# Kernel optimization log

Measured on AMD Instinct MI355X. Metric: run time of the kernel, lower is better.

Reference implementation:

```python
import jax, jax.numpy as jnp
import numpy as np

N = 50000      # nodes
IN = 128       # in_channels
H = 8          # heads
C = 16         # out_channels per head (128 // 8)
E = 800000     # edges per relation
R = 2          # number of relations
NEG_SLOPE = 0.2


def setup_inputs() -> dict:
    key = jax.random.key(0)
    ks = jax.random.split(key, 6)
    x = jax.random.normal(ks[0], (N, IN), jnp.float32)
    edge_index0 = jax.random.randint(ks[1], (2, E), 0, N, jnp.int32)
    edge_index1 = jax.random.randint(ks[2], (2, E), 0, N, jnp.int32)
    s_in = np.float32(1.0 / np.sqrt(IN))
    Wl = jax.random.normal(ks[3], (R, IN, H * C), jnp.float32) * s_in
    Wr = jax.random.normal(ks[4], (R, IN, H * C), jnp.float32) * s_in
    att = jax.random.normal(ks[5], (R, H, C), jnp.float32) * np.float32(1.0 / np.sqrt(C))
    bl = jnp.zeros((R, H * C), jnp.float32)
    br = jnp.zeros((R, H * C), jnp.float32)
    bias = jnp.zeros((R, H * C), jnp.float32)
    return dict(x=x, edge_index0=edge_index0, edge_index1=edge_index1,
                Wl=Wl, bl=bl, Wr=Wr, br=br, att=att, bias=bias)


def _gatv2_conv(x, edge_index, Wl, bl, Wr, br, att, bias):
    """One PyG-style GATv2Conv (share_weights=False, add_self_loops=True, concat=True)."""
    loops = jnp.arange(N, dtype=edge_index.dtype)
    src = jnp.concatenate([edge_index[0], loops])  # [E+N]
    dst = jnp.concatenate([edge_index[1], loops])  # [E+N]
    xl = (x @ Wl + bl).reshape(N, H, C)  # source-side transform (messages)
    xr = (x @ Wr + br).reshape(N, H, C)  # destination-side transform
    # GATv2 attention: att . leaky_relu(x_l[src] + x_r[dst])
    e = jax.nn.leaky_relu(xl[src] + xr[dst], NEG_SLOPE)        # [E+N, H, C]
    score = jnp.einsum('ehc,hc->eh', e, att)                   # [E+N, H]
    # per-destination softmax (numerically stable via segment max)
    m = jax.ops.segment_max(score, dst, num_segments=N)        # [N, H]
    m = jax.lax.stop_gradient(jnp.where(jnp.isfinite(m), m, jnp.zeros_like(m)))
    ex = jnp.exp(score - m[dst])
    den = jax.ops.segment_sum(ex, dst, num_segments=N)         # [N, H]
    alpha = ex / den[dst]                                      # [E+N, H]
    # scatter-add weighted source messages
    out = jax.ops.segment_sum(alpha[:, :, None] * xl[src], dst, num_segments=N)  # [N, H, C]
    return out.reshape(N, H * C) + bias


def reference(x, edge_index0, edge_index1, Wl, bl, Wr, br, att, bias):
    eis = (edge_index0, edge_index1)
    out = jnp.zeros((N, H * C), x.dtype)
    for r in range(R):  # small fixed loop over relation types
        out = out + _gatv2_conv(x, eis[r], Wl[r], bl[r], Wr[r], br[r], att[r], bias[r])
    return out
```

## Files before the change

### kernel.cpp

```cpp
#include <hip/hip_runtime.h>
#include <math.h>

#define NN 50000
#define EE 800000
#define NB 196
#define BCAP 6250
#define LCAP 32

typedef __attribute__((ext_vector_type(8))) short bf16x8;
typedef __attribute__((ext_vector_type(4))) float f32x4;

__device__ inline uint bfpack(float a, float b) {
    uint ua = __float_as_uint(a); ua = (ua + 0x7FFFu + ((ua >> 16) & 1u)) >> 16;
    uint ub = __float_as_uint(b); ub = (ub + 0x7FFFu + ((ub >> 16) & 1u)) >> 16;
    return ua | (ub << 16);
}

__global__ __launch_bounds__(256) void k_prep(
    const float* __restrict__ x, const float* __restrict__ Wl, const float* __restrict__ Wr,
    ushort* __restrict__ xb, ushort* __restrict__ wt, int* __restrict__ gcur)
{
    int i = blockIdx.x * 256 + threadIdx.x;
    if (i < NN * 32) {
        float4 v = ((const float4*)x)[i];
        uint2 p; p.x = bfpack(v.x, v.y); p.y = bfpack(v.z, v.w);
        ((uint2*)xb)[i] = p;
    }
    if (i < 4 * 16384) {
        int c = i >> 14, rem = i & 16383, nn = rem >> 7, k = rem & 127;
        const float* W = ((c & 1) ? Wr : Wl) + (c >> 1) * 16384;
        float v = W[k * 128 + nn];
        uint u = __float_as_uint(v); u = (u + 0x7FFFu + ((u >> 16) & 1u)) >> 16;
        wt[c * 16384 + nn * 128 + k] = (ushort)u;
    }
    if (i < 2 * 256 * 16) gcur[i] = 0;
}

__global__ __launch_bounds__(256) void k_gemm_all(
    const ushort* __restrict__ xb, const ushort* __restrict__ wt,
    const float* __restrict__ bl, const float* __restrict__ br,
    ushort* __restrict__ xall)
{
    const int c = blockIdx.y;
    const ushort* __restrict__ w = wt + c * 16384;
    const float* __restrict__ bv = ((c & 1) ? br : bl) + (c >> 1) * 128;
    ushort* __restrict__ outp = xall + (size_t)c * NN * 128;

    const int wid = threadIdx.x >> 6, lane = threadIdx.x & 63;
    const int hi = lane >> 4, lo = lane & 15;
    const int row = blockIdx.x * 64 + wid * 16 + lo;
    const int rc = (row < NN) ? row : NN - 1;

    f32x4 acc[8];
    #pragma unroll
    for (int tt = 0; tt < 8; ++tt) acc[tt] = (f32x4){0.f, 0.f, 0.f, 0.f};

    #pragma unroll
    for (int kk = 0; kk < 128; kk += 32) {
        bf16x8 bfr = *(const bf16x8*)&xb[(size_t)rc * 128 + kk + hi * 8];
        #pragma unroll
        for (int tt = 0; tt < 8; ++tt) {
            bf16x8 afr = *(const bf16x8*)&w[(tt * 16 + lo) * 128 + kk + hi * 8];
            acc[tt] = __builtin_amdgcn_mfma_f32_16x16x32_bf16(afr, bfr, acc[tt], 0, 0, 0);
        }
    }
    if (row < NN) {
        #pragma unroll
        for (int tt = 0; tt < 8; ++tt) {
            float4 bvv = *(const float4*)&bv[tt * 16 + hi * 4];
            uint2 pk;
            pk.x = bfpack(acc[tt][0] + bvv.x, acc[tt][1] + bvv.y);
            pk.y = bfpack(acc[tt][2] + bvv.z, acc[tt][3] + bvv.w);
            *(uint2*)&outp[(size_t)row * 128 + tt * 16 + hi * 4] = pk;
        }
    }
}

__global__ __launch_bounds__(256) void k_bin1(
    const int* __restrict__ ei0, const int* __restrict__ ei1,
    int* __restrict__ gcur, uint* __restrict__ gbuf)
{
    const int rel = blockIdx.y;
    const int* __restrict__ ei = rel ? ei1 : ei0;
    int* __restrict__ gc = gcur + rel * 256 * 16;
    uint* __restrict__ gb = gbuf + (size_t)rel * 256 * BCAP;

    __shared__ uint stage[256 * LCAP];
    __shared__ int scnt[256];
    const int tid = threadIdx.x;
    scnt[tid] = 0;
    __syncthreads();

    const int base = blockIdx.x * 2048;
    uint keys[8]; int bk[8];
    #pragma unroll
    for (int k = 0; k < 8; ++k) {
        int e = base + tid + k * 256;
        bool v = (e < EE);
        int d = v ? ei[EE + e] : 0;
        int s = v ? ei[e] : 0;
        keys[k] = ((uint)d << 16) | (uint)s;
        bk[k] = v ? (d >> 8) : -1;
    }
    #pragma unroll
    for (int k = 0; k < 8; ++k) {
        if (bk[k] >= 0) {
            int pos = atomicAdd(&scnt[bk[k]], 1);
            if (pos < LCAP) stage[bk[k] * LCAP + pos] = keys[k];
            else {
                int gpos = atomicAdd(&gc[bk[k] * 16], 1);
                if (gpos < BCAP) gb[bk[k] * BCAP + gpos] = keys[k];
            }
        }
    }
    __syncthreads();
    int c = scnt[tid]; if (c > LCAP) c = LCAP;
    if (c > 0) {
        int b0 = atomicAdd(&gc[tid * 16], c);
        if (b0 + c > BCAP) c = (b0 < BCAP) ? (BCAP - b0) : 0;
        for (int i = 0; i < c; ++i) gb[tid * BCAP + b0 + i] = stage[tid * LCAP + i];
    }
}

__global__ __launch_bounds__(256) void k_bin2(
    const int* __restrict__ gcur, const uint* __restrict__ gbuf,
    ushort* __restrict__ bin0, ushort* __restrict__ bin1,
    int* __restrict__ cur0, int* __restrict__ cur1)
{
    const int rel = blockIdx.y;
    const int b = blockIdx.x;
    const int* __restrict__ gc = gcur + rel * 256 * 16;
    const uint* __restrict__ gb = gbuf + (size_t)rel * 256 * BCAP + (size_t)b * BCAP;
    ushort* __restrict__ bins = rel ? bin1 : bin0;
    int* __restrict__ cur = rel ? cur1 : cur0;

    __shared__ int cnt[256];
    cnt[threadIdx.x] = 0;
    __syncthreads();
    int n = gc[b * 16]; if (n > BCAP) n = BCAP;
    for (int i = threadIdx.x; i < n; i += 256) {
        uint key = gb[i];
        int d = key >> 16;
        int pos = atomicAdd(&cnt[d & 255], 1);
        if (pos < 64) bins[(size_t)d * 64 + pos] = (ushort)(key & 0xFFFF);
    }
    __syncthreads();
    int gd = (b << 8) + threadIdx.x;
    if (gd < NN) cur[gd] = cnt[threadIdx.x];
}

__global__ __launch_bounds__(256) void k_gat(
    const ushort* __restrict__ xall,
    const int* __restrict__ cur0, const int* __restrict__ cur1,
    const ushort* __restrict__ bin0, const ushort* __restrict__ bin1,
    const float* __restrict__ att, const float* __restrict__ bias,
    float* __restrict__ out)
{
    const int wid  = threadIdx.x >> 6;
    const int lane = threadIdx.x & 63;
    const int li   = lane & 31;
    const int half = lane >> 5;
    const int d = blockIdx.x * 4 + wid;

    const uint2* __restrict__ x2 = (const uint2*)xall;
    const size_t hb = (size_t)(half * 2) * NN * 32;
    const size_t rb = (size_t)(half * 2 + 1) * NN * 32;

    float4 av = *(const float4*)&att[half * 128 + li * 4];
    uint2 ur = x2[rb + (size_t)d * 32 + li];
    float r0 = __uint_as_float(ur.x << 16), r1 = __uint_as_float(ur.x & 0xFFFF0000u);
    float r2 = __uint_as_float(ur.y << 16), r3 = __uint_as_float(ur.y & 0xFFFF0000u);

    int nb = (half ? cur1 : cur0)[d]; nb = (nb > 64) ? 64 : nb;
    const int n = nb + 1;
    int nm = n;
    nm = max(nm, __shfl_xor(nm, 32));
    const ushort* __restrict__ brow = (half ? bin1 : bin0) + (size_t)d * 64;

    auto sidx = [&](int e) -> int {
        int ec = (e < n) ? e : (n - 1);
        return (ec == 0) ? d : (int)brow[ec - 1];
    };

    uint2 u0 = x2[hb + (size_t)sidx(0) * 32 + li];
    uint2 u1 = x2[hb + (size_t)sidx(1) * 32 + li];
    int   s2 = sidx(2);

    float a0 = 0.f, a1 = 0.f, a2 = 0.f, a3 = 0.f, den = 0.f;
    for (int t = 0; t < nm; ++t) {
        uint2 cu = u0;
        u0 = u1;
        u1 = x2[hb + (size_t)s2 * 32 + li];
        s2 = sidx(t + 3);
        float c0 = __uint_as_float(cu.x << 16), c1 = __uint_as_float(cu.x & 0xFFFF0000u);
        float c2 = __uint_as_float(cu.y << 16), c3 = __uint_as_float(cu.y & 0xFFFF0000u);
        float q0 = c0 + r0, q1 = c1 + r1, q2 = c2 + r2, q3 = c3 + r3;
        q0 = fmaxf(q0, 0.2f * q0); q1 = fmaxf(q1, 0.2f * q1);
        q2 = fmaxf(q2, 0.2f * q2); q3 = fmaxf(q3, 0.2f * q3);
        float p = av.x * q0 + av.y * q1 + av.z * q2 + av.w * q3;
        p += __shfl_xor(p, 1);
        p += __shfl_xor(p, 2);
        float ex = (t < n) ? __expf(p) : 0.f;
        a0 += ex * c0; a1 += ex * c1; a2 += ex * c2; a3 += ex * c3; den += ex;
    }
    float inv = 1.f / den;
    float b0 = a0 * inv, b1 = a1 * inv, b2 = a2 * inv, b3 = a3 * inv;
    b0 += __shfl_xor(b0, 32);
    b1 += __shfl_xor(b1, 32);
    b2 += __shfl_xor(b2, 32);
    b3 += __shfl_xor(b3, 32);
    if (half == 0) {
        float4 bb0 = *(const float4*)&bias[li * 4];
        float4 bb1 = *(const float4*)&bias[128 + li * 4];
        float4 o;
        o.x = bb0.x + bb1.x + b0; o.y = bb0.y + bb1.y + b1;
        o.z = bb0.z + bb1.z + b2; o.w = bb0.w + bb1.w + b3;
        *(float4*)&out[(size_t)d * 128 + li * 4] = o;
    }
}

extern "C" void kernel_launch(void* const* d_in, const int* in_sizes, int n_in,
                              void* d_out, int out_size, void* d_ws, size_t ws_size,
                              hipStream_t stream) {
    (void)in_sizes; (void)n_in; (void)out_size; (void)ws_size;
    const float* x    = (const float*)d_in[0];
    const int*   ei0  = (const int*)  d_in[1];
    const int*   ei1  = (const int*)  d_in[2];
    const float* Wl   = (const float*)d_in[3];
    const float* bl   = (const float*)d_in[4];
    const float* Wr   = (const float*)d_in[5];
    const float* br   = (const float*)d_in[6];
    const float* att  = (const float*)d_in[7];
    const float* bias = (const float*)d_in[8];
    float* out = (float*)d_out;

    ushort* xb   = (ushort*)d_ws;
    uint*   gbuf = (uint*)d_ws;
    ushort* wt   = xb + (size_t)NN * 128;
    ushort* xall = wt + 4 * 16384;
    ushort* bin0 = xall + (size_t)4 * NN * 128;
    ushort* bin1 = bin0 + (size_t)NN * 64;
    int* cur0 = (int*)(bin1 + (size_t)NN * 64);
    int* cur1 = cur0 + NN;
    int* gcur = cur1 + NN;

    k_prep<<<(NN * 32 + 255) / 256, 256, 0, stream>>>(x, Wl, Wr, xb, wt, gcur);
    k_gemm_all<<<dim3((NN + 63) / 64, 4), 256, 0, stream>>>(xb, wt, bl, br, xall);
    k_bin1<<<dim3((EE + 2047) / 2048, 2), 256, 0, stream>>>(ei0, ei1, gcur, gbuf);
    k_bin2<<<dim3(NB, 2), 256, 0, stream>>>(gcur, gbuf, bin0, bin1, cur0, cur1);
    k_gat<<<NN / 4, 256, 0, stream>>>(xall, cur0, cur1, bin0, bin1, att, bias, out);
}
```

Before: 265.3 us.

## Fuse x conversion into GEMM, precompute attention dots, simplify GAT score math

Converts x to bf16 inside the GEMM instead of in a separate prep pass, and has the GEMM also emit per-head att·x dot products. The GAT kernel splits leaky_relu into a linear part taken from the precomputed dots plus an abs term, and uses exp2 with folded log2e constants and 32-bit index arithmetic. The bin flush in k_bin1 becomes wave-cooperative, with one atomic per bucket and parallel lane writes. This adds an extra dotv gather per edge and a larger workspace footprint.

```diff
diff --git a/kernel.cpp b/kernel.cpp
--- a/kernel.cpp
+++ b/kernel.cpp
@@ -15,17 +15,14 @@
     uint ub = __float_as_uint(b); ub = (ub + 0x7FFFu + ((ub >> 16) & 1u)) >> 16;
     return ua | (ub << 16);
 }
+__device__ inline float bflo(uint u) { return __uint_as_float(u << 16); }
+__device__ inline float bfhi(uint u) { return __uint_as_float(u & 0xFFFF0000u); }
 
 __global__ __launch_bounds__(256) void k_prep(
-    const float* __restrict__ x, const float* __restrict__ Wl, const float* __restrict__ Wr,
-    ushort* __restrict__ xb, ushort* __restrict__ wt, int* __restrict__ gcur)
+    const float* __restrict__ Wl, const float* __restrict__ Wr,
+    ushort* __restrict__ wt, int* __restrict__ gcur)
 {
     int i = blockIdx.x * 256 + threadIdx.x;
-    if (i < NN * 32) {
-        float4 v = ((const float4*)x)[i];
-        uint2 p; p.x = bfpack(v.x, v.y); p.y = bfpack(v.z, v.w);
-        ((uint2*)xb)[i] = p;
-    }
     if (i < 4 * 16384) {
         int c = i >> 14, rem = i & 16383, nn = rem >> 7, k = rem & 127;
         const float* W = ((c & 1) ? Wr : Wl) + (c >> 1) * 16384;
@@ -37,14 +34,17 @@
 }
 
 __global__ __launch_bounds__(256) void k_gemm_all(
-    const ushort* __restrict__ xb, const ushort* __restrict__ wt,
+    const float* __restrict__ x, const ushort* __restrict__ wt,
     const float* __restrict__ bl, const float* __restrict__ br,
-    ushort* __restrict__ xall)
+    const float* __restrict__ att,
+    ushort* __restrict__ xall, float* __restrict__ dotv)
 {
     const int c = blockIdx.y;
     const ushort* __restrict__ w = wt + c * 16384;
     const float* __restrict__ bv = ((c & 1) ? br : bl) + (c >> 1) * 128;
+    const float* __restrict__ attp = att + (c >> 1) * 128;
     ushort* __restrict__ outp = xall + (size_t)c * NN * 128;
+    float* __restrict__ dvp = dotv + (size_t)c * NN * 8;
 
     const int wid = threadIdx.x >> 6, lane = threadIdx.x & 63;
     const int hi = lane >> 4, lo = lane & 15;
@@ -57,7 +57,12 @@
 
     #pragma unroll
     for (int kk = 0; kk < 128; kk += 32) {
-        bf16x8 bfr = *(const bf16x8*)&xb[(size_t)rc * 128 + kk + hi * 8];
+        const float4* xp = (const float4*)&x[(size_t)rc * 128 + kk + hi * 8];
+        float4 f0 = xp[0], f1 = xp[1];
+        uint4 px;
+        px.x = bfpack(f0.x, f0.y); px.y = bfpack(f0.z, f0.w);
+        px.z = bfpack(f1.x, f1.y); px.w = bfpack(f1.z, f1.w);
+        bf16x8 bfr = *(bf16x8*)&px;
         #pragma unroll
         for (int tt = 0; tt < 8; ++tt) {
             bf16x8 afr = *(const bf16x8*)&w[(tt * 16 + lo) * 128 + kk + hi * 8];
@@ -72,6 +77,12 @@
             pk.x = bfpack(acc[tt][0] + bvv.x, acc[tt][1] + bvv.y);
             pk.y = bfpack(acc[tt][2] + bvv.z, acc[tt][3] + bvv.w);
             *(uint2*)&outp[(size_t)row * 128 + tt * 16 + hi * 4] = pk;
+            float w0 = bflo(pk.x), w1 = bfhi(pk.x), w2 = bflo(pk.y), w3 = bfhi(pk.y);
+            float4 a4 = *(const float4*)&attp[tt * 16 + hi * 4];
+            float s = a4.x * w0 + a4.y * w1 + a4.z * w2 + a4.w * w3;
+            s += __shfl_xor(s, 16);
+            s += __shfl_xor(s, 32);
+            if (hi == 0) dvp[(size_t)row * 8 + tt] = s;
         }
     }
 }
@@ -114,11 +125,19 @@
         }
     }
     __syncthreads();
-    int c = scnt[tid]; if (c > LCAP) c = LCAP;
-    if (c > 0) {
-        int b0 = atomicAdd(&gc[tid * 16], c);
-        if (b0 + c > BCAP) c = (b0 < BCAP) ? (BCAP - b0) : 0;
-        for (int i = 0; i < c; ++i) gb[tid * BCAP + b0 + i] = stage[tid * LCAP + i];
+    const int wv = tid >> 6, ln = tid & 63;
+    #pragma unroll 4
+    for (int g = 0; g < 64; ++g) {
+        int b = wv * 64 + g;
+        int cnum = scnt[b]; if (cnum > LCAP) cnum = LCAP;
+        if (cnum == 0) continue;
+        int b0 = 0;
+        if (ln == 0) b0 = atomicAdd(&gc[b * 16], cnum);
+        b0 = __shfl(b0, 0);
+        if (ln < cnum) {
+            int idx = b0 + ln;
+            if (idx < BCAP) gb[b * BCAP + idx] = stage[b * LCAP + ln];
+        }
     }
 }
 
@@ -150,7 +169,7 @@
 }
 
 __global__ __launch_bounds__(256) void k_gat(
-    const ushort* __restrict__ xall,
+    const ushort* __restrict__ xall, const float* __restrict__ dotv,
     const int* __restrict__ cur0, const int* __restrict__ cur1,
     const ushort* __restrict__ bin0, const ushort* __restrict__ bin1,
     const float* __restrict__ att, const float* __restrict__ bias,
@@ -160,16 +179,24 @@
     const int lane = threadIdx.x & 63;
     const int li   = lane & 31;
     const int half = lane >> 5;
+    const int h    = li >> 2;
     const int d = blockIdx.x * 4 + wid;
 
     const uint2* __restrict__ x2 = (const uint2*)xall;
-    const size_t hb = (size_t)(half * 2) * NN * 32;
-    const size_t rb = (size_t)(half * 2 + 1) * NN * 32;
-
+    const uint hb = (uint)(half * 2) * (NN * 32);
+    const uint rb = hb + NN * 32;
+    const float* __restrict__ dAp = dotv + (size_t)(half * 2) * NN * 8;
+    const float* __restrict__ dBp = dAp + (size_t)NN * 8;
+
+    const float L2E = 1.4426950408889634f;
+    const float C6 = 0.6f * L2E;
     float4 av = *(const float4*)&att[half * 128 + li * 4];
-    uint2 ur = x2[rb + (size_t)d * 32 + li];
-    float r0 = __uint_as_float(ur.x << 16), r1 = __uint_as_float(ur.x & 0xFFFF0000u);
-    float r2 = __uint_as_float(ur.y << 16), r3 = __uint_as_float(ur.y & 0xFFFF0000u);
+    const float k4 = 0.4f * L2E;
+    float avx = av.x * k4, avy = av.y * k4, avz = av.z * k4, avw = av.w * k4;
+
+    uint2 ur = x2[rb + (uint)d * 32 + li];
+    float r0 = bflo(ur.x), r1 = bfhi(ur.x), r2 = bflo(ur.y), r3 = bfhi(ur.y);
+    float dBk = C6 * dBp[(uint)d * 8 + h];
 
     int nb = (half ? cur1 : cur0)[d]; nb = (nb > 64) ? 64 : nb;
     const int n = nb + 1;
@@ -182,26 +209,33 @@
         return (ec == 0) ? d : (int)brow[ec - 1];
     };
 
-    uint2 u0 = x2[hb + (size_t)sidx(0) * 32 + li];
-    uint2 u1 = x2[hb + (size_t)sidx(1) * 32 + li];
-    int   s2 = sidx(2);
+    int s0i = sidx(0), s1i = sidx(1);
+    uint2 u0 = x2[hb + (uint)s0i * 32 + li];
+    float g0 = dAp[(uint)s0i * 8 + h];
+    uint2 u1 = x2[hb + (uint)s1i * 32 + li];
+    float g1 = dAp[(uint)s1i * 8 + h];
+    int s2 = sidx(2);
 
     float a0 = 0.f, a1 = 0.f, a2 = 0.f, a3 = 0.f, den = 0.f;
     for (int t = 0; t < nm; ++t) {
-        uint2 cu = u0;
-        u0 = u1;
-        u1 = x2[hb + (size_t)s2 * 32 + li];
+        uint2 cu = u0; float cg = g0;
+        u0 = u1; g0 = g1;
+        u1 = x2[hb + (uint)s2 * 32 + li];
+        g1 = dAp[(uint)s2 * 8 + h];
         s2 = sidx(t + 3);
-        float c0 = __uint_as_float(cu.x << 16), c1 = __uint_as_float(cu.x & 0xFFFF0000u);
-        float c2 = __uint_as_float(cu.y << 16), c3 = __uint_as_float(cu.y & 0xFFFF0000u);
+        float c0 = bflo(cu.x), c1 = bfhi(cu.x), c2 = bflo(cu.y), c3 = bfhi(cu.y);
         float q0 = c0 + r0, q1 = c1 + r1, q2 = c2 + r2, q3 = c3 + r3;
-        q0 = fmaxf(q0, 0.2f * q0); q1 = fmaxf(q1, 0.2f * q1);
-        q2 = fmaxf(q2, 0.2f * q2); q3 = fmaxf(q3, 0.2f * q3);
-        float p = av.x * q0 + av.y * q1 + av.z * q2 + av.w * q3;
-        p += __shfl_xor(p, 1);
-        p += __shfl_xor(p, 2);
-        float ex = (t < n) ? __expf(p) : 0.f;
-        a0 += ex * c0; a1 += ex * c1; a2 += ex * c2; a3 += ex * c3; den += ex;
+        float m = avx * fabsf(q0);
+        m = fmaf(avy, fabsf(q1), m);
+        m = fmaf(avz, fabsf(q2), m);
+        m = fmaf(avw, fabsf(q3), m);
+        m += __shfl_xor(m, 1);
+        m += __shfl_xor(m, 2);
+        float p = m + fmaf(C6, cg, dBk);
+        float ex = (t < n) ? __builtin_amdgcn_exp2f(p) : 0.f;
+        a0 = fmaf(ex, c0, a0); a1 = fmaf(ex, c1, a1);
+        a2 = fmaf(ex, c2, a2); a3 = fmaf(ex, c3, a3);
+        den += ex;
     }
     float inv = 1.f / den;
     float b0 = a0 * inv, b1 = a1 * inv, b2 = a2 * inv, b3 = a3 * inv;
@@ -234,19 +268,19 @@
     const float* bias = (const float*)d_in[8];
     float* out = (float*)d_out;
 
-    ushort* xb   = (ushort*)d_ws;
-    uint*   gbuf = (uint*)d_ws;
-    ushort* wt   = xb + (size_t)NN * 128;
-    ushort* xall = wt + 4 * 16384;
-    ushort* bin0 = xall + (size_t)4 * NN * 128;
+    ushort* xall = (ushort*)d_ws;
+    float*  dotv = (float*)(xall + (size_t)4 * NN * 128);
+    uint*   gbuf = (uint*)(dotv + (size_t)4 * NN * 8);
+    ushort* wt   = (ushort*)(gbuf + (size_t)2 * 256 * BCAP);
+    ushort* bin0 = wt + 4 * 16384;
     ushort* bin1 = bin0 + (size_t)NN * 64;
     int* cur0 = (int*)(bin1 + (size_t)NN * 64);
     int* cur1 = cur0 + NN;
     int* gcur = cur1 + NN;
 
-    k_prep<<<(NN * 32 + 255) / 256, 256, 0, stream>>>(x, Wl, Wr, xb, wt, gcur);
-    k_gemm_all<<<dim3((NN + 63) / 64, 4), 256, 0, stream>>>(xb, wt, bl, br, xall);
+    k_prep<<<256, 256, 0, stream>>>(Wl, Wr, wt, gcur);
+    k_gemm_all<<<dim3((NN + 63) / 64, 4), 256, 0, stream>>>(x, wt, bl, br, att, xall, dotv);
     k_bin1<<<dim3((EE + 2047) / 2048, 2), 256, 0, stream>>>(ei0, ei1, gcur, gbuf);
     k_bin2<<<dim3(NB, 2), 256, 0, stream>>>(gcur, gbuf, bin0, bin1, cur0, cur1);
-    k_gat<<<NN / 4, 256, 0, stream>>>(xall, cur0, cur1, bin0, bin1, att, bias, out);
-}
+    k_gat<<<NN / 4, 256, 0, stream>>>(xall, dotv, cur0, cur1, bin0, bin1, att, bias, out);
+}
```

Result: slower. 315.1 us (+18.8%).
